# Optimization experiments

Measured on AMD Instinct MI355X. Metric: run time of the kernel, lower is better.

## Reference

```python
import jax, jax.numpy as jnp
import numpy as np


def setup_inputs() -> dict:
    key = jax.random.key(0)
    ks = jax.random.split(key, 6)
    B, T, D, U = 128, 1024, 256, 256
    x = jax.random.normal(ks[0], (B, T, D), jnp.float32)
    s = lambda k, sh: jax.random.normal(k, sh, jnp.float32) * 0.05
    W_zr = s(ks[1], (D, 2 * U))
    U_zr = s(ks[2], (U, 2 * U))
    # bias_initializer: zeros for update gate, ones for reset gate
    b_zr = jnp.concatenate([jnp.zeros((U,), jnp.float32), jnp.ones((U,), jnp.float32)])
    W_h = s(ks[3], (D, U))
    U_h = s(ks[4], (U, U))
    b_h = jnp.zeros((U,), jnp.float32)
    return {"x": x, "W_zr": W_zr, "U_zr": U_zr, "b_zr": b_zr,
            "W_h": W_h, "U_h": U_h, "b_h": b_h}


def reference(x, W_zr, U_zr, b_zr, W_h, U_h, b_h):
    B, T, D = x.shape
    U = W_h.shape[1]
    # Precompute input-side projections for all timesteps (math-equivalent,
    # batches the per-step Dense(ip) matmuls into two big GEMMs).
    xz = jnp.einsum('btd,de->bte', x, W_zr)   # [B,T,2U]
    xh = jnp.einsum('btd,du->btu', x, W_h)    # [B,T,U]

    def step(h, inp):
        xz_t, xh_t = inp                       # [B,2U], [B,U]
        z = xz_t + h @ U_zr + b_zr
        Z = jax.nn.sigmoid(z[:, :U])           # update gate
        R = jax.nn.sigmoid(z[:, U:2 * U])      # reset gate
        S_ = jnp.tanh(xh_t + (R * h) @ U_h + b_h)
        h_new = (1.0 - Z) * h + Z * S_
        return h_new, None

    h0 = jnp.zeros((B, U), x.dtype)
    h_last, _ = jax.lax.scan(step, h0,
                             (jnp.swapaxes(xz, 0, 1), jnp.swapaxes(xh, 0, 1)))
    # return_sequence=False, return_states=False -> last hidden state [B,U]
    return h_last
```

## Files before the change

### kernel.cpp

```cpp
#include <hip/hip_runtime.h>
#include <hip/hip_bf16.h>
#include <cstdint>
#include <cstddef>

#define B_ 128
#define T_ 1024
#define D_ 256
#define U_ 256

typedef __bf16 bfrag __attribute__((ext_vector_type(8)));
typedef unsigned short us8 __attribute__((ext_vector_type(8)));
typedef unsigned short us4 __attribute__((ext_vector_type(4)));
typedef float f32x4 __attribute__((ext_vector_type(4)));

#define SC_ZR (-1.4426950408889634f)
#define SC_H  (2.8853900817779268f)

__device__ __forceinline__ unsigned short f2bf(float f) {
    unsigned int u = __builtin_bit_cast(unsigned int, f);
    unsigned int r = (u + 0x7fffu + ((u >> 16) & 1u)) >> 16;
    return (unsigned short)r;
}
__device__ __forceinline__ float bf2f(unsigned short h) {
    unsigned int u = ((unsigned int)h) << 16;
    return __builtin_bit_cast(float, u);
}
__device__ __forceinline__ unsigned int pk_bf16(float lo, float hi) {
    unsigned int d;
    asm("v_cvt_pk_bf16_f32 %0, %1, %2" : "=v"(d) : "v"(lo), "v"(hi));
    return d;
}
__device__ __forceinline__ unsigned int pk_hu(float lo, float hi) {
    unsigned int a = __builtin_bit_cast(unsigned int, lo) + 0x8000u;
    unsigned int b = __builtin_bit_cast(unsigned int, hi) + 0x8000u;
#if __has_builtin(__builtin_amdgcn_perm)
    return __builtin_amdgcn_perm(b, a, 0x07060302u);
#else
    return (b & 0xffff0000u) | (a >> 16);
#endif
}

#if __has_builtin(__builtin_amdgcn_exp2f)
__device__ __forceinline__ float fexp2(float x) { return __builtin_amdgcn_exp2f(x); }
#else
__device__ __forceinline__ float fexp2(float x) { return exp2f(x); }
#endif
#if __has_builtin(__builtin_amdgcn_rcpf)
__device__ __forceinline__ float frcp(float x) { return __builtin_amdgcn_rcpf(x); }
#else
__device__ __forceinline__ float frcp(float x) { return 1.0f / x; }
#endif

__device__ __forceinline__ float sigm_pre(float zp) {
    return frcp(1.0f + fexp2(zp));
}
__device__ __forceinline__ float tanh_pre(float sp) {
    return 1.0f - 2.0f * frcp(1.0f + fexp2(sp));
}

#define BARRIER_LGKM() asm volatile("s_waitcnt lgkmcnt(0)\n\ts_barrier" ::: "memory")

#define TSTR2 3072
#define GSTR  ((size_t)T_ * TSTR2)
#define WTSZ  (768 * 256)

__global__ __launch_bounds__(64) void wt_kernel(
    const float* __restrict__ Wzr, const float* __restrict__ Wh,
    unsigned short* __restrict__ Wt, int ncopies)
{
    const int c = blockIdx.x;
    const int lane = threadIdx.x;
    const float* Wp; int ldw, cc;
    if (c < 512) { Wp = Wzr; ldw = 512; cc = c; }
    else         { Wp = Wh;  ldw = 256; cc = c - 512; }
    const float sc = (c < 512) ? SC_ZR : SC_H;
    const int k0 = lane * 4;
    const float a = sc * Wp[(size_t)(k0 + 0) * ldw + cc];
    const float b = sc * Wp[(size_t)(k0 + 1) * ldw + cc];
    const float d = sc * Wp[(size_t)(k0 + 2) * ldw + cc];
    const float e = sc * Wp[(size_t)(k0 + 3) * ldw + cc];
    uint2 u; u.x = pk_bf16(a, b); u.y = pk_bf16(d, e);
    for (int r = 0; r < ncopies; ++r)
        *reinterpret_cast<uint2*>(&Wt[(size_t)r * WTSZ + (size_t)c * 256 + k0]) = u;
}

#define LPA 264

__global__ __launch_bounds__(256, 4) void proj_kernel(
    const float* __restrict__ x, const unsigned short* __restrict__ Wt,
    const float* __restrict__ bzr, const float* __restrict__ bh,
    unsigned short* __restrict__ xzh, size_t wtstride)
{
    const int tid  = threadIdx.x;
    const int lane = tid & 63;
    const int wv   = tid >> 6;
    const int q    = lane >> 4;
    const int c16  = lane & 15;
    const int bb = blockIdx.x >> 8;
    const int tb = blockIdx.x & 255;

    __shared__ __align__(16) unsigned short ldsA[64 * LPA];

    {
        const int r0 = wv * 16;
#pragma unroll
        for (int r = 0; r < 16; ++r) {
            const int row = r0 + r;
            const float* xr = x + (((size_t)(bb * 16 + (row & 15))) * T_
                                   + tb * 4 + (row >> 4)) * D_;
            f32x4 v = *reinterpret_cast<const f32x4*>(xr + lane * 4);
            uint2 u; u.x = pk_bf16(v[0], v[1]); u.y = pk_bf16(v[2], v[3]);
            *reinterpret_cast<uint2*>(&ldsA[row * LPA + lane * 4]) = u;
        }
    }
    __syncthreads();

    const int R0 = (wv >> 1) * 32;
    us8 af[2][8];
#pragma unroll
    for (int m2 = 0; m2 < 2; ++m2)
#pragma unroll
        for (int kk = 0; kk < 8; ++kk)
            af[m2][kk] = *reinterpret_cast<const us8*>(
                &ldsA[(R0 + m2 * 16 + c16) * LPA + kk * 32 + q * 8]);

    const int wn = wv & 1;
    const unsigned short* p0 = Wt + (size_t)bb * wtstride
                               + ((size_t)(wn * 32 + c16) * 256 + q * 8);
    const unsigned short* p1 = p0 + 16 * 256;

#pragma unroll 1
    for (int ch = 0; ch < 12; ++ch) {
        f32x4 acc[2][2] = {};
#pragma unroll
        for (int kk = 0; kk < 8; ++kk) {
            us8 w0 = *reinterpret_cast<const us8*>(p0 + kk * 32);
            us8 w1 = *reinterpret_cast<const us8*>(p1 + kk * 32);
#pragma unroll
            for (int m2 = 0; m2 < 2; ++m2) {
                acc[m2][0] = __builtin_amdgcn_mfma_f32_16x16x32_bf16(
                    __builtin_bit_cast(bfrag, af[m2][kk]), __builtin_bit_cast(bfrag, w0),
                    acc[m2][0], 0, 0, 0);
                acc[m2][1] = __builtin_amdgcn_mfma_f32_16x16x32_bf16(
                    __builtin_bit_cast(bfrag, af[m2][kk]), __builtin_bit_cast(bfrag, w1),
                    acc[m2][1], 0, 0, 0);
            }
        }
#pragma unroll
        for (int n2 = 0; n2 < 2; ++n2) {
            const int gcn = ch * 64 + wn * 32 + n2 * 16 + c16;
            const float bias = (gcn < 512) ? (SC_ZR * bzr[gcn])
                                           : (SC_H * bh[gcn - 512]);
#pragma unroll
            for (int m2 = 0; m2 < 2; ++m2) {
                const int t = tb * 4 + (wv >> 1) * 2 + m2;
                uint2 uu;
                uu.x = pk_bf16(acc[m2][n2][0] + bias, acc[m2][n2][1] + bias);
                uu.y = pk_bf16(acc[m2][n2][2] + bias, acc[m2][n2][3] + bias);
                *reinterpret_cast<uint2*>(
                    &xzh[((((size_t)(bb * 4 + q)) * T_ + t) * 768 + gcn) * 4]) = uu;
            }
        }
        p0 += 64 * 256; p1 += 64 * 256;
    }
}

#define HBP 272
#define HB4 (4 * HBP)

__global__ __launch_bounds__(512, 2) void gru_rec(
    const float* __restrict__ Uzr, const float* __restrict__ Uh,
    const unsigned short* __restrict__ xzh, float* __restrict__ out)
{
    const int tid  = threadIdx.x;
    const int lane = tid & 63;
    const int w    = tid >> 6;
    const int q    = lane >> 4;
    const int c16  = lane & 15;
    const int g    = blockIdx.x;

    __shared__ __align__(16) unsigned short hb[2 * HB4];
    __shared__ __align__(16) unsigned short rhb[HB4];

    us8 wA[4][8];
#pragma unroll
    for (int nt = 0; nt < 4; ++nt) {
        const int col = (nt < 2) ? (w * 32 + nt * 16 + c16)
                                 : (256 + w * 32 + (nt - 2) * 16 + c16);
#pragma unroll
        for (int kk = 0; kk < 8; ++kk) {
            us8 v;
#pragma unroll
            for (int j = 0; j < 8; ++j) {
                const int kr = kk * 32 + q * 4 + (j >> 1) + 16 * (j & 1);
                v[j] = f2bf(SC_ZR * Uzr[(size_t)kr * 512 + col]);
            }
            wA[nt][kk] = v;
        }
    }
    us8 wB[2][8];
#pragma unroll
    for (int nt = 0; nt < 2; ++nt) {
        const int col = w * 32 + nt * 16 + c16;
#pragma unroll
        for (int kk = 0; kk < 8; ++kk) {
            us8 v;
#pragma unroll
            for (int j = 0; j < 8; ++j) {
                const int kr = kk * 32 + q * 4 + (j >> 1) + 16 * (j & 1);
                v[j] = f2bf(SC_H * Uh[(size_t)kr * 256 + col]);
            }
            wB[nt][kk] = v;
        }
    }

    for (int i = tid; i < 2 * HB4; i += 512) hb[i] = 0;
    for (int i = tid; i < HB4; i += 512) rhb[i] = 0;
    __syncthreads();

    float h0 = 0.0f, h1 = 0.0f;

    size_t laneA[4], laneB[2];
#pragma unroll
    for (int nt = 0; nt < 4; ++nt) {
        const int col = (nt < 2) ? (w * 32 + nt * 16 + c16)
                                 : (256 + w * 32 + (nt - 2) * 16 + c16);
        laneA[nt] = (size_t)g * GSTR + (size_t)col * 4 + q;
    }
#pragma unroll
    for (int nt = 0; nt < 2; ++nt)
        laneB[nt] = (size_t)g * GSTR
                    + (size_t)(512 + w * 32 + nt * 16 + c16) * 4 + q;

    unsigned short ca[4], cxh[2];
#pragma unroll
    for (int nt = 0; nt < 4; ++nt) ca[nt] = xzh[laneA[nt]];
#pragma unroll
    for (int nt = 0; nt < 2; ++nt) cxh[nt] = xzh[laneB[nt]];

    size_t toff = TSTR2;

    const int dwr = q * HBP + w * 32 + 2 * c16;
    const int ard = (c16 >> 2) * HBP + q * 8;

    int rb = 0;

#pragma unroll 1
    for (int t = 0; t < T_; ++t) {
        const int wb = rb ^ HB4;
        unsigned short na[4], nxh[2];
#pragma unroll
        for (int nt = 0; nt < 4; ++nt) na[nt] = xzh[laneA[nt] + toff];
#pragma unroll
        for (int nt = 0; nt < 2; ++nt) nxh[nt] = xzh[laneB[nt] + toff];
        if (t < 1022) toff += TSTR2;

        us8 afr[8];
#pragma unroll
        for (int kk = 0; kk < 8; ++kk)
            afr[kk] = *reinterpret_cast<const us8*>(&hb[rb + ard + kk * 32]);

        f32x4 accR[2];
#pragma unroll
        for (int nt = 0; nt < 2; ++nt) {
            const float v = bf2f(ca[2 + nt]);
            accR[nt][0] = v; accR[nt][1] = v; accR[nt][2] = v; accR[nt][3] = v;
        }
#pragma unroll
        for (int kk = 0; kk < 8; ++kk) {
            bfrag af = __builtin_bit_cast(bfrag, afr[kk]);
            accR[0] = __builtin_amdgcn_mfma_f32_16x16x32_bf16(
                af, __builtin_bit_cast(bfrag, wA[2][kk]), accR[0], 0, 0, 0);
            accR[1] = __builtin_amdgcn_mfma_f32_16x16x32_bf16(
                af, __builtin_bit_cast(bfrag, wA[3][kk]), accR[1], 0, 0, 0);
        }
        {
            const float r0 = sigm_pre(accR[0][0]);
            const float r1 = sigm_pre(accR[1][0]);
            *reinterpret_cast<unsigned int*>(&rhb[dwr]) = pk_hu(r0 * h0, r1 * h1);
        }

        f32x4 accZ[2];
#pragma unroll
        for (int nt = 0; nt < 2; ++nt) {
            const float v = bf2f(ca[nt]);
            accZ[nt][0] = v; accZ[nt][1] = v; accZ[nt][2] = v; accZ[nt][3] = v;
        }
#pragma unroll
        for (int kk = 0; kk < 8; ++kk) {
            bfrag af = __builtin_bit_cast(bfrag, afr[kk]);
            accZ[0] = __builtin_amdgcn_mfma_f32_16x16x32_bf16(
                af, __builtin_bit_cast(bfrag, wA[0][kk]), accZ[0], 0, 0, 0);
            accZ[1] = __builtin_amdgcn_mfma_f32_16x16x32_bf16(
                af, __builtin_bit_cast(bfrag, wA[1][kk]), accZ[1], 0, 0, 0);
        }
        BARRIER_LGKM();

        f32x4 acc2[2];
#pragma unroll
        for (int nt = 0; nt < 2; ++nt) {
            const float v = bf2f(cxh[nt]);
            acc2[nt][0] = v; acc2[nt][1] = v; acc2[nt][2] = v; acc2[nt][3] = v;
        }
#pragma unroll
        for (int kk = 0; kk < 8; ++kk) {
            bfrag rf = __builtin_bit_cast(bfrag,
                *reinterpret_cast<const us8*>(&rhb[ard + kk * 32]));
            acc2[0] = __builtin_amdgcn_mfma_f32_16x16x32_bf16(
                rf, __builtin_bit_cast(bfrag, wB[0][kk]), acc2[0], 0, 0, 0);
            acc2[1] = __builtin_amdgcn_mfma_f32_16x16x32_bf16(
                rf, __builtin_bit_cast(bfrag, wB[1][kk]), acc2[1], 0, 0, 0);
        }
        {
            const float z0 = sigm_pre(accZ[0][0]);
            const float z1 = sigm_pre(accZ[1][0]);
            const float s0 = tanh_pre(acc2[0][0]);
            const float s1 = tanh_pre(acc2[1][0]);
            h0 = fmaf(z0, s0 - h0, h0);
            h1 = fmaf(z1, s1 - h1, h1);
            *reinterpret_cast<unsigned int*>(&hb[wb + dwr]) = pk_hu(h0, h1);
        }
#pragma unroll
        for (int nt = 0; nt < 4; ++nt) ca[nt] = na[nt];
#pragma unroll
        for (int nt = 0; nt < 2; ++nt) cxh[nt] = nxh[nt];
        BARRIER_LGKM();
        rb = wb;
    }

    out[(size_t)(g * 4 + q) * 256 + w * 32 + c16] = h0;
    out[(size_t)(g * 4 + q) * 256 + w * 32 + 16 + c16] = h1;
}

extern "C" void kernel_launch(void* const* d_in, const int* in_sizes, int n_in,
                              void* d_out, int out_size, void* d_ws, size_t ws_size,
                              hipStream_t stream) {
    const float* x   = (const float*)d_in[0];
    const float* Wzr = (const float*)d_in[1];
    const float* Uzr = (const float*)d_in[2];
    const float* bzr = (const float*)d_in[3];
    const float* Wh  = (const float*)d_in[4];
    const float* Uh  = (const float*)d_in[5];
    const float* bh  = (const float*)d_in[6];
    float* out = (float*)d_out;

    const size_t xzhbytes = (size_t)32 * GSTR * 2;
    const size_t wtbytes  = (size_t)WTSZ * 2;
    int ncopies = (ws_size >= xzhbytes + 8 * wtbytes) ? 8
                : (ws_size >= xzhbytes + wtbytes) ? 1 : 1;
    unsigned short* xzh = (unsigned short*)d_ws;
    unsigned short* Wt  = (unsigned short*)((char*)d_ws + xzhbytes);
    const size_t wtstride = (ncopies == 8) ? (size_t)WTSZ : 0;

    wt_kernel<<<dim3(768), dim3(64), 0, stream>>>(Wzr, Wh, Wt, ncopies);
    proj_kernel<<<dim3(2048), dim3(256), 0, stream>>>(x, Wt, bzr, bh, xzh, wtstride);
    gru_rec<<<dim3(32), dim3(512), 0, stream>>>(Uzr, Uh, xzh, out);
}
```

Measured before the change: 1.697 ms.

## Fuse projection and recurrence into one kernel with flag-based producer-consumer sync

Merges the input projection GEMM and the sequential GRU recurrence into a single launch. The first 32 blocks run the recurrence and the remaining 1024 blocks compute projections for 8-timestep chunks, each publishing a release flag when its chunk is written. Recurrence blocks spin on acquire loads of these flags before reading each chunk. This lets the long serial recurrence start while projections are still being produced, instead of waiting for the whole projection kernel. The cost is a flag memset, spin-waiting, and a reliance on the low-numbered recurrence blocks being co-resident with the producers so the spin-wait cannot deadlock.

```diff
diff --git a/kernel.cpp b/kernel.cpp
--- a/kernel.cpp
+++ b/kernel.cpp
@@ -10,7 +10,6 @@
 
 typedef __bf16 bfrag __attribute__((ext_vector_type(8)));
 typedef unsigned short us8 __attribute__((ext_vector_type(8)));
-typedef unsigned short us4 __attribute__((ext_vector_type(4)));
 typedef float f32x4 __attribute__((ext_vector_type(4)));
 
 #define SC_ZR (-1.4426950408889634f)
@@ -85,99 +84,110 @@
 }
 
 #define LPA 264
-
-__global__ __launch_bounds__(256, 4) void proj_kernel(
+#define HBP 272
+#define HB4 (4 * HBP)
+
+__global__ __launch_bounds__(512, 2) void fused_kernel(
     const float* __restrict__ x, const unsigned short* __restrict__ Wt,
     const float* __restrict__ bzr, const float* __restrict__ bh,
-    unsigned short* __restrict__ xzh, size_t wtstride)
+    unsigned short* __restrict__ xzh, size_t wtstride,
+    const float* __restrict__ Uzr, const float* __restrict__ Uh,
+    float* __restrict__ out, unsigned int* __restrict__ flags)
 {
-    const int tid  = threadIdx.x;
-    const int lane = tid & 63;
-    const int wv   = tid >> 6;
-    const int q    = lane >> 4;
-    const int c16  = lane & 15;
-    const int bb = blockIdx.x >> 8;
-    const int tb = blockIdx.x & 255;
-
-    __shared__ __align__(16) unsigned short ldsA[64 * LPA];
-
-    {
-        const int r0 = wv * 16;
-#pragma unroll
-        for (int r = 0; r < 16; ++r) {
-            const int row = r0 + r;
-            const float* xr = x + (((size_t)(bb * 16 + (row & 15))) * T_
-                                   + tb * 4 + (row >> 4)) * D_;
-            f32x4 v = *reinterpret_cast<const f32x4*>(xr + lane * 4);
-            uint2 u; u.x = pk_bf16(v[0], v[1]); u.y = pk_bf16(v[2], v[3]);
-            *reinterpret_cast<uint2*>(&ldsA[row * LPA + lane * 4]) = u;
-        }
-    }
-    __syncthreads();
-
-    const int R0 = (wv >> 1) * 32;
-    us8 af[2][8];
-#pragma unroll
-    for (int m2 = 0; m2 < 2; ++m2)
-#pragma unroll
-        for (int kk = 0; kk < 8; ++kk)
-            af[m2][kk] = *reinterpret_cast<const us8*>(
-                &ldsA[(R0 + m2 * 16 + c16) * LPA + kk * 32 + q * 8]);
-
-    const int wn = wv & 1;
-    const unsigned short* p0 = Wt + (size_t)bb * wtstride
-                               + ((size_t)(wn * 32 + c16) * 256 + q * 8);
-    const unsigned short* p1 = p0 + 16 * 256;
+    const int bid = blockIdx.x;
+    const int tid = threadIdx.x;
+
+    if (bid >= 32) {
+        const int p    = bid - 32;
+        const int tb8  = p >> 3;
+        const int bb   = p & 7;
+        const int lane = tid & 63;
+        const int wv8  = tid >> 6;
+        const int gidx = wv8 >> 2;
+        const int wl   = wv8 & 3;
+        const int q    = lane >> 4;
+        const int c16  = lane & 15;
+        const int tbe  = tb8 * 2 + gidx;
+
+        __shared__ __align__(16) unsigned short ldsA[2][64 * LPA];
+
+        {
+            const int r0 = wl * 16;
+#pragma unroll
+            for (int r = 0; r < 16; ++r) {
+                const int row = r0 + r;
+                const float* xr = x + (((size_t)(bb * 16 + (row & 15))) * T_
+                                       + tbe * 4 + (row >> 4)) * D_;
+                f32x4 v = *reinterpret_cast<const f32x4*>(xr + lane * 4);
+                uint2 u; u.x = pk_bf16(v[0], v[1]); u.y = pk_bf16(v[2], v[3]);
+                *reinterpret_cast<uint2*>(&ldsA[gidx][row * LPA + lane * 4]) = u;
+            }
+        }
+        __syncthreads();
+
+        const int R0 = (wl >> 1) * 32;
+        us8 af[2][8];
+#pragma unroll
+        for (int m2 = 0; m2 < 2; ++m2)
+#pragma unroll
+            for (int kk = 0; kk < 8; ++kk)
+                af[m2][kk] = *reinterpret_cast<const us8*>(
+                    &ldsA[gidx][(R0 + m2 * 16 + c16) * LPA + kk * 32 + q * 8]);
+
+        const int wn = wl & 1;
+        const unsigned short* p0 = Wt + (size_t)bb * wtstride
+                                   + ((size_t)(wn * 32 + c16) * 256 + q * 8);
+        const unsigned short* p1 = p0 + 16 * 256;
 
 #pragma unroll 1
-    for (int ch = 0; ch < 12; ++ch) {
-        f32x4 acc[2][2] = {};
-#pragma unroll
-        for (int kk = 0; kk < 8; ++kk) {
-            us8 w0 = *reinterpret_cast<const us8*>(p0 + kk * 32);
-            us8 w1 = *reinterpret_cast<const us8*>(p1 + kk * 32);
-#pragma unroll
-            for (int m2 = 0; m2 < 2; ++m2) {
-                acc[m2][0] = __builtin_amdgcn_mfma_f32_16x16x32_bf16(
-                    __builtin_bit_cast(bfrag, af[m2][kk]), __builtin_bit_cast(bfrag, w0),
-                    acc[m2][0], 0, 0, 0);
-                acc[m2][1] = __builtin_amdgcn_mfma_f32_16x16x32_bf16(
-                    __builtin_bit_cast(bfrag, af[m2][kk]), __builtin_bit_cast(bfrag, w1),
-                    acc[m2][1], 0, 0, 0);
-            }
-        }
-#pragma unroll
-        for (int n2 = 0; n2 < 2; ++n2) {
-            const int gcn = ch * 64 + wn * 32 + n2 * 16 + c16;
-            const float bias = (gcn < 512) ? (SC_ZR * bzr[gcn])
-                                           : (SC_H * bh[gcn - 512]);
-#pragma unroll
-            for (int m2 = 0; m2 < 2; ++m2) {
-                const int t = tb * 4 + (wv >> 1) * 2 + m2;
-                uint2 uu;
-                uu.x = pk_bf16(acc[m2][n2][0] + bias, acc[m2][n2][1] + bias);
-                uu.y = pk_bf16(acc[m2][n2][2] + bias, acc[m2][n2][3] + bias);
-                *reinterpret_cast<uint2*>(
-                    &xzh[((((size_t)(bb * 4 + q)) * T_ + t) * 768 + gcn) * 4]) = uu;
-            }
-        }
-        p0 += 64 * 256; p1 += 64 * 256;
-    }
-}
-
-#define HBP 272
-#define HB4 (4 * HBP)
-
-__global__ __launch_bounds__(512, 2) void gru_rec(
-    const float* __restrict__ Uzr, const float* __restrict__ Uh,
-    const unsigned short* __restrict__ xzh, float* __restrict__ out)
-{
-    const int tid  = threadIdx.x;
+        for (int ch = 0; ch < 12; ++ch) {
+            f32x4 acc[2][2] = {};
+#pragma unroll
+            for (int kk = 0; kk < 8; ++kk) {
+                us8 w0 = *reinterpret_cast<const us8*>(p0 + kk * 32);
+                us8 w1 = *reinterpret_cast<const us8*>(p1 + kk * 32);
+#pragma unroll
+                for (int m2 = 0; m2 < 2; ++m2) {
+                    acc[m2][0] = __builtin_amdgcn_mfma_f32_16x16x32_bf16(
+                        __builtin_bit_cast(bfrag, af[m2][kk]), __builtin_bit_cast(bfrag, w0),
+                        acc[m2][0], 0, 0, 0);
+                    acc[m2][1] = __builtin_amdgcn_mfma_f32_16x16x32_bf16(
+                        __builtin_bit_cast(bfrag, af[m2][kk]), __builtin_bit_cast(bfrag, w1),
+                        acc[m2][1], 0, 0, 0);
+                }
+            }
+#pragma unroll
+            for (int n2 = 0; n2 < 2; ++n2) {
+                const int gcn = ch * 64 + wn * 32 + n2 * 16 + c16;
+                const float bias = (gcn < 512) ? (SC_ZR * bzr[gcn])
+                                               : (SC_H * bh[gcn - 512]);
+#pragma unroll
+                for (int m2 = 0; m2 < 2; ++m2) {
+                    const int t = tbe * 4 + (wl >> 1) * 2 + m2;
+                    uint2 uu;
+                    uu.x = pk_bf16(acc[m2][n2][0] + bias, acc[m2][n2][1] + bias);
+                    uu.y = pk_bf16(acc[m2][n2][2] + bias, acc[m2][n2][3] + bias);
+                    *reinterpret_cast<uint2*>(
+                        &xzh[((((size_t)(bb * 4 + q)) * T_ + t) * 768 + gcn) * 4]) = uu;
+                }
+            }
+            p0 += 64 * 256; p1 += 64 * 256;
+        }
+
+        __threadfence();
+        __syncthreads();
+        if (tid == 0)
+            __hip_atomic_store(&flags[bb * 128 + tb8], 1u,
+                               __ATOMIC_RELEASE, __HIP_MEMORY_SCOPE_AGENT);
+        return;
+    }
+
     const int lane = tid & 63;
     const int w    = tid >> 6;
     const int q    = lane >> 4;
     const int c16  = lane & 15;
-    const int g    = blockIdx.x;
+    const int g    = bid;
+    const unsigned int* fl = flags + (g >> 2) * 128;
 
     __shared__ __align__(16) unsigned short hb[2 * HB4];
     __shared__ __align__(16) unsigned short rhb[HB4];
@@ -232,6 +242,11 @@
         laneB[nt] = (size_t)g * GSTR
                     + (size_t)(512 + w * 32 + nt * 16 + c16) * 4 + q;
 
+    unsigned int sl_ok = 0;
+    while (__hip_atomic_load(&fl[0], __ATOMIC_ACQUIRE,
+                             __HIP_MEMORY_SCOPE_AGENT) == 0) {}
+    sl_ok = 1;
+
     unsigned short ca[4], cxh[2];
 #pragma unroll
     for (int nt = 0; nt < 4; ++nt) ca[nt] = xzh[laneA[nt]];
@@ -248,6 +263,14 @@
 #pragma unroll 1
     for (int t = 0; t < T_; ++t) {
         const int wb = rb ^ HB4;
+        if (t < 1023) {
+            const unsigned int s1 = (unsigned int)(t + 1) >> 3;
+            if (s1 >= sl_ok) {
+                while (__hip_atomic_load(&fl[s1], __ATOMIC_ACQUIRE,
+                                         __HIP_MEMORY_SCOPE_AGENT) == 0) {}
+                sl_ok = s1 + 1;
+            }
+        }
         unsigned short na[4], nxh[2];
 #pragma unroll
         for (int nt = 0; nt < 4; ++nt) na[nt] = xzh[laneA[nt] + toff];
@@ -268,11 +291,11 @@
         }
 #pragma unroll
         for (int kk = 0; kk < 8; ++kk) {
-            bfrag af = __builtin_bit_cast(bfrag, afr[kk]);
+            bfrag af2 = __builtin_bit_cast(bfrag, afr[kk]);
             accR[0] = __builtin_amdgcn_mfma_f32_16x16x32_bf16(
-                af, __builtin_bit_cast(bfrag, wA[2][kk]), accR[0], 0, 0, 0);
+                af2, __builtin_bit_cast(bfrag, wA[2][kk]), accR[0], 0, 0, 0);
             accR[1] = __builtin_amdgcn_mfma_f32_16x16x32_bf16(
-                af, __builtin_bit_cast(bfrag, wA[3][kk]), accR[1], 0, 0, 0);
+                af2, __builtin_bit_cast(bfrag, wA[3][kk]), accR[1], 0, 0, 0);
         }
         {
             const float r0 = sigm_pre(accR[0][0]);
@@ -288,11 +311,11 @@
         }
 #pragma unroll
         for (int kk = 0; kk < 8; ++kk) {
-            bfrag af = __builtin_bit_cast(bfrag, afr[kk]);
+            bfrag af2 = __builtin_bit_cast(bfrag, afr[kk]);
             accZ[0] = __builtin_amdgcn_mfma_f32_16x16x32_bf16(
-                af, __builtin_bit_cast(bfrag, wA[0][kk]), accZ[0], 0, 0, 0);
+                af2, __builtin_bit_cast(bfrag, wA[0][kk]), accZ[0], 0, 0, 0);
             accZ[1] = __builtin_amdgcn_mfma_f32_16x16x32_bf16(
-                af, __builtin_bit_cast(bfrag, wA[1][kk]), accZ[1], 0, 0, 0);
+                af2, __builtin_bit_cast(bfrag, wA[1][kk]), accZ[1], 0, 0, 0);
         }
         BARRIER_LGKM();
 
@@ -345,14 +368,16 @@
     float* out = (float*)d_out;
 
     const size_t xzhbytes = (size_t)32 * GSTR * 2;
+    const size_t flagbytes = 4096;
     const size_t wtbytes  = (size_t)WTSZ * 2;
-    int ncopies = (ws_size >= xzhbytes + 8 * wtbytes) ? 8
-                : (ws_size >= xzhbytes + wtbytes) ? 1 : 1;
     unsigned short* xzh = (unsigned short*)d_ws;
-    unsigned short* Wt  = (unsigned short*)((char*)d_ws + xzhbytes);
+    unsigned int* flags = (unsigned int*)((char*)d_ws + xzhbytes);
+    unsigned short* Wt  = (unsigned short*)((char*)d_ws + xzhbytes + flagbytes);
+    int ncopies = (ws_size >= xzhbytes + flagbytes + 8 * wtbytes) ? 8 : 1;
     const size_t wtstride = (ncopies == 8) ? (size_t)WTSZ : 0;
 
     wt_kernel<<<dim3(768), dim3(64), 0, stream>>>(Wzr, Wh, Wt, ncopies);
-    proj_kernel<<<dim3(2048), dim3(256), 0, stream>>>(x, Wt, bzr, bh, xzh, wtstride);
-    gru_rec<<<dim3(32), dim3(512), 0, stream>>>(Uzr, Uh, xzh, out);
-}
+    hipMemsetAsync(flags, 0, flagbytes, stream);
+    fused_kernel<<<dim3(1056), dim3(512), 0, stream>>>(
+        x, Wt, bzr, bh, xzh, wtstride, Uzr, Uh, out, flags);
+}
```

New measurement: 1.720 ms. Within noise of the previous version (+1.4%).
